# Performance work log

Hardware: AMD Instinct MI355X
Metric: run time of the kernel (lower is better)

## Reference

```python
import jax, jax.numpy as jnp
import numpy as np

N = 10000
E = 160000
C = 256        # in_channels
M = 256        # mid_channels
R = 64         # nregion


def _glorot(key, shape):
    fan_in, fan_out = shape[-1], shape[0]
    lim = (6.0 / (fan_in + fan_out)) ** 0.5
    return jax.random.uniform(key, shape, jnp.float32, -lim, lim)


def setup_inputs() -> dict:
    key = jax.random.key(0)
    ks = jax.random.split(key, 12)
    x = jax.random.normal(ks[0], (N, C), jnp.float32)
    edge_index = jax.random.randint(ks[1], (2, E), 0, N, jnp.int32)
    conv_w = _glorot(ks[2], (C, C))
    conv_b = jnp.zeros((C,), jnp.float32)
    lin1_w = _glorot(ks[3], (M, C)); lin1_b = jnp.zeros((M,), jnp.float32)
    lin2_w = _glorot(ks[4], (M, M)); lin2_b = jnp.zeros((M,), jnp.float32)
    lin3_w = _glorot(ks[5], (1, M)); lin3_b = jnp.zeros((1,), jnp.float32)
    lin4_w = _glorot(ks[6], (M, M)); lin4_b = jnp.zeros((M,), jnp.float32)
    bilin_w = _glorot(ks[7], (R, M, M)) * 0.1
    bilin_b = jnp.zeros((R,), jnp.float32)
    return {"x": x, "edge_index": edge_index,
            "conv_w": conv_w, "conv_b": conv_b,
            "lin1_w": lin1_w, "lin1_b": lin1_b,
            "lin2_w": lin2_w, "lin2_b": lin2_b,
            "lin3_w": lin3_w, "lin3_b": lin3_b,
            "lin4_w": lin4_w, "lin4_b": lin4_b,
            "bilin_w": bilin_w, "bilin_b": bilin_b}


def gcn_conv(x, edge_index, w, b):
    # PyG GCNConv: add self-loops, symmetric D^-1/2 (A+I) D^-1/2 normalization
    src, dst = edge_index[0], edge_index[1]
    n = x.shape[0]
    xw = x @ w.T                                            # [N, C]
    deg = jnp.ones((n,), xw.dtype).at[dst].add(jnp.ones((E,), xw.dtype))  # +1 for self loop
    dinv = jax.lax.rsqrt(deg)
    norm = dinv[src] * dinv[dst]                            # [E]
    agg = jnp.zeros_like(xw).at[dst].add(norm[:, None] * xw[src])
    agg = agg + (dinv * dinv)[:, None] * xw                 # self-loop messages
    return agg + b


def reference(x, edge_index, conv_w, conv_b, lin1_w, lin1_b, lin2_w, lin2_b,
              lin3_w, lin3_b, lin4_w, lin4_b, bilin_w, bilin_b):
    out = jax.nn.relu(gcn_conv(x, edge_index, conv_w, conv_b))
    x0 = out + x                                            # residual [N, C]
    x0 = jax.nn.relu(x0 @ lin1_w.T + lin1_b)                # [N, M]
    x1 = jax.nn.relu(x0 @ lin2_w.T + lin2_b)
    x1 = x1 @ lin3_w.T + lin3_b                             # [N, 1]
    x2 = jax.nn.relu(x0 @ lin4_w.T + lin4_b)                # [N, M]
    # Bilinear(x2, x2): out[n,r] = x2[n] @ W[r] @ x2[n] + b[r]
    t = (x2 @ bilin_w.reshape(R * M, M).T).reshape(-1, R, M)  # [N, R, M]
    x2 = jnp.sum(t * x2[:, None, :], axis=-1) + bilin_b       # [N, R]
    return (x1, x2)
```

## Files before the change

### kernel.cpp

```cpp
#include <hip/hip_runtime.h>

typedef unsigned short u16;
typedef __attribute__((ext_vector_type(8))) short bf16x8;
typedef __attribute__((ext_vector_type(8))) unsigned short u16x8;
typedef __attribute__((ext_vector_type(4))) float f32x4;

#define N_NODES 10000
#define E_EDGES 160000
#define CX_N 2560000
#define W_N  65536
#define WB_N 4194304
#define CANON_BIG_BLOCKS 3426
#define HIST_BLOCKS 79

__device__ __forceinline__ float b2f(u16 u) {
  union { unsigned i; float f; } c; c.i = ((unsigned)u) << 16; return c.f;
}
__device__ __forceinline__ u16 f2b(float f) {
  union { float f; unsigned i; } c; c.f = f;
  unsigned i = c.i;
  return (u16)((i + 0x7FFFu + ((i >> 16) & 1u)) >> 16);
}

__global__ void detect_kernel(const unsigned* __restrict__ w, int* __restrict__ flag) {
  int t = threadIdx.x;
  int cnt = 0;
  for (int i = t; i < 1024; i += 64) {
    unsigned e = (w[i] >> 7) & 0xFF;
    cnt += (e >= 100 && e <= 145) ? 1 : 0;
  }
  for (int o = 32; o; o >>= 1) cnt += __shfl_xor(cnt, o);
  if (t == 0) *flag = (cnt >= 512) ? 1 : 0;
}

__global__ void canon_all_kernel(const void* sx, const void* swc, const void* sw1,
                                 const void* sw2, const void* sw4, const void* swB,
                                 const void* sbc, const void* sb1, const void* sb2,
                                 const void* sb4, const void* sw3, const void* sbB,
                                 const void* sb3,
                                 u16* __restrict__ dstBase,
                                 u16* cbc, u16* cb1, u16* cb2, u16* cb4,
                                 u16* cw3, u16* cbB, u16* cb3,
                                 const int* __restrict__ ei, int* __restrict__ count,
                                 const int* __restrict__ flag) {
  int b = blockIdx.x;
  int f = *flag;
  if (b < CANON_BIG_BLOCKS) {
    long e = ((long)b * 256 + threadIdx.x) * 8;
    const void* src; long so;
    if (e < CX_N)                { src = sx;  so = e; }
    else if (e < CX_N + W_N)     { src = swc; so = e - CX_N; }
    else if (e < CX_N + 2 * W_N) { src = sw1; so = e - (CX_N + W_N); }
    else if (e < CX_N + 3 * W_N) { src = sw2; so = e - (CX_N + 2 * W_N); }
    else if (e < CX_N + 4 * W_N) { src = sw4; so = e - (CX_N + 3 * W_N); }
    else                         { src = swB; so = e - (CX_N + 4 * W_N); }
    if (f) {
      u16x8 v = *((const u16x8*)((const u16*)src + so));
      *(u16x8*)(dstBase + e) = v;
    } else {
      const float* fp = (const float*)src + so;
      float4 a = *(const float4*)fp;
      float4 c = *(const float4*)(fp + 4);
      u16x8 o;
      o[0] = f2b(a.x); o[1] = f2b(a.y); o[2] = f2b(a.z); o[3] = f2b(a.w);
      o[4] = f2b(c.x); o[5] = f2b(c.y); o[6] = f2b(c.z); o[7] = f2b(c.w);
      *(u16x8*)(dstBase + e) = o;
    }
  } else if (b == CANON_BIG_BLOCKS) {
    int t = threadIdx.x;
    const void* srcs[7] = {sbc, sb1, sb2, sb4, sw3, sbB, sb3};
    u16* dsts[7] = {cbc, cb1, cb2, cb4, cw3, cbB, cb3};
    const int ns[7] = {256, 256, 256, 256, 256, 64, 1};
#pragma unroll
    for (int k = 0; k < 7; ++k) {
      if (t < ns[k]) {
        if (f) dsts[k][t] = ((const u16*)srcs[k])[t];
        else   dsts[k][t] = f2b(((const float*)srcs[k])[t]);
      }
    }
  } else {
    int base = (b - CANON_BIG_BLOCKS - 1) * 2048 + threadIdx.x * 8;
#pragma unroll
    for (int k = 0; k < 8; ++k) {
      int i = base + k;
      if (i < E_EDGES) atomicAdd(&count[ei[E_EDGES + i]], 1);
    }
  }
}

__device__ __forceinline__ void stage_async(const u16* __restrict__ src, int stride,
                                            int row0, int maxRow, int k0,
                                            u16* lds, int w, int lane) {
  int rsel = lane >> 3;
  int gch = (lane & 7) ^ rsel;
#pragma unroll
  for (int i = 0; i < 4; ++i) {
    int rb = (w * 4 + i) * 8;
    int grow = row0 + rb + rsel;
    grow = grow > maxRow ? maxRow : grow;
    const u16* gp = src + (size_t)grow * stride + k0 + gch * 8;
    u16* lp = lds + rb * 64;
    __builtin_amdgcn_global_load_lds(
        (const __attribute__((address_space(1))) void*)gp,
        (__attribute__((address_space(3))) void*)lp, 16, 0, 0);
  }
}

__device__ __forceinline__ void mma_tile(const u16* lA, const u16* lB,
                                         f32x4 acc[4][4], int wr, int wc, int lane) {
#pragma unroll
  for (int ks = 0; ks < 2; ++ks) {
    bf16x8 af[4], bfr[4];
    int g = ks * 4 + (lane >> 4);
#pragma unroll
    for (int t = 0; t < 4; ++t) {
      int rowA = wr * 64 + t * 16 + (lane & 15);
      af[t] = *(const bf16x8*)(lA + rowA * 64 + ((g ^ (rowA & 7)) * 8));
      int rowB = wc * 64 + t * 16 + (lane & 15);
      bfr[t] = *(const bf16x8*)(lB + rowB * 64 + ((g ^ (rowB & 7)) * 8));
    }
#pragma unroll
    for (int ti = 0; ti < 4; ++ti)
#pragma unroll
      for (int tj = 0; tj < 4; ++tj)
        acc[ti][tj] = __builtin_amdgcn_mfma_f32_16x16x32_bf16(af[ti], bfr[tj],
                                                              acc[ti][tj], 0, 0, 0);
  }
}

template <bool RELU, bool F32OUT>
__global__ __launch_bounds__(256, 2)
void gemm_kernel(const u16* __restrict__ A, const u16* __restrict__ B,
                 const u16* __restrict__ bias, float* __restrict__ outF,
                 u16* __restrict__ outB, int NN, int J, int K) {
  __shared__ u16 lA[128 * 64];
  __shared__ u16 lB[128 * 64];
  int lane = threadIdx.x & 63;
  int w = threadIdx.x >> 6;
  int wr = w >> 1, wc = w & 1;
  int n0 = blockIdx.y * 128;
  int j0 = blockIdx.x * 128;
  f32x4 acc[4][4];
#pragma unroll
  for (int i = 0; i < 4; ++i)
#pragma unroll
    for (int j = 0; j < 4; ++j) acc[i][j] = (f32x4){0.f, 0.f, 0.f, 0.f};

  for (int kt = 0; kt < K; kt += 64) {
    stage_async(A, K, n0, NN - 1, kt, lA, w, lane);
    stage_async(B, K, j0, J - 1, kt, lB, w, lane);
    __syncthreads();
    mma_tile(lA, lB, acc, wr, wc, lane);
    __syncthreads();
  }

#pragma unroll
  for (int ti = 0; ti < 4; ++ti)
#pragma unroll
    for (int tj = 0; tj < 4; ++tj) {
      int col = j0 + wc * 64 + tj * 16 + (lane & 15);
      float bv = bias ? b2f(bias[col]) : 0.0f;
#pragma unroll
      for (int r = 0; r < 4; ++r) {
        int row = n0 + wr * 64 + ti * 16 + ((lane >> 4) << 2) + r;
        if (row < NN) {
          float v = acc[ti][tj][r] + bv;
          if (RELU) v = fmaxf(v, 0.0f);
          if (F32OUT) outF[(size_t)row * J + col] = v;
          else        outB[(size_t)row * J + col] = f2b(v);
        }
      }
    }
}

__global__ __launch_bounds__(256, 2)
void gemm_fused234_kernel(const u16* __restrict__ A, const u16* __restrict__ B,
                          const u16* __restrict__ bias, const u16* __restrict__ w3,
                          float* __restrict__ out1acc, u16* __restrict__ x2v, int NN) {
  __shared__ u16 lA[128 * 64];
  __shared__ u16 lB[128 * 64];
  int lane = threadIdx.x & 63;
  int w = threadIdx.x >> 6;
  int wr = w >> 1, wc = w & 1;
  int n0 = blockIdx.y * 128;
  int j0 = blockIdx.x * 128;
  f32x4 acc[4][4];
#pragma unroll
  for (int i = 0; i < 4; ++i)
#pragma unroll
    for (int j = 0; j < 4; ++j) acc[i][j] = (f32x4){0.f, 0.f, 0.f, 0.f};

  for (int kt = 0; kt < 256; kt += 64) {
    stage_async(A, 256, n0, NN - 1, kt, lA, w, lane);
    stage_async(B, 256, j0, 511, kt, lB, w, lane);
    __syncthreads();
    mma_tile(lA, lB, acc, wr, wc, lane);
    __syncthreads();
  }

  if (j0 < 256) {
    float part[4][4];
#pragma unroll
    for (int ti = 0; ti < 4; ++ti)
#pragma unroll
      for (int r = 0; r < 4; ++r) part[ti][r] = 0.0f;
#pragma unroll
    for (int ti = 0; ti < 4; ++ti)
#pragma unroll
      for (int tj = 0; tj < 4; ++tj) {
        int col = j0 + wc * 64 + tj * 16 + (lane & 15);
        float bv = b2f(bias[col]);
        float wv = b2f(w3[col]);
#pragma unroll
        for (int r = 0; r < 4; ++r) {
          float v = fmaxf(acc[ti][tj][r] + bv, 0.0f);
          part[ti][r] += v * wv;
        }
      }
#pragma unroll
    for (int ti = 0; ti < 4; ++ti)
#pragma unroll
      for (int r = 0; r < 4; ++r) {
        float s = part[ti][r];
        s += __shfl_xor(s, 1);
        s += __shfl_xor(s, 2);
        s += __shfl_xor(s, 4);
        s += __shfl_xor(s, 8);
        if ((lane & 15) == 0) {
          int row = n0 + wr * 64 + ti * 16 + ((lane >> 4) << 2) + r;
          if (row < NN) unsafeAtomicAdd(&out1acc[row], s);
        }
      }
  } else {
#pragma unroll
    for (int ti = 0; ti < 4; ++ti)
#pragma unroll
      for (int tj = 0; tj < 4; ++tj) {
        int col = j0 + wc * 64 + tj * 16 + (lane & 15);
        float bv = b2f(bias[col]);
#pragma unroll
        for (int r = 0; r < 4; ++r) {
          int row = n0 + wr * 64 + ti * 16 + ((lane >> 4) << 2) + r;
          if (row < NN) {
            float v = fmaxf(acc[ti][tj][r] + bv, 0.0f);
            x2v[(size_t)row * 256 + (col - 256)] = f2b(v);
          }
        }
      }
  }
}

__global__ __launch_bounds__(256, 2)
void bilinear_kernel(const u16* __restrict__ x2v, const u16* __restrict__ W,
                     float* __restrict__ out2acc, int NN) {
  __shared__ u16 lA[128 * 64];
  __shared__ u16 lB[128 * 64];
  int lane = threadIdx.x & 63;
  int w = threadIdx.x >> 6;
  int wr = w >> 1, wc = w & 1;
  int n0 = blockIdx.y * 128;
  int rm0 = blockIdx.x * 128;
  int m0g = rm0 & 255;
  int xv_kt = (m0g >> 6) + wc;
  f32x4 acc[4][4];
#pragma unroll
  for (int i = 0; i < 4; ++i)
#pragma unroll
    for (int j = 0; j < 4; ++j) acc[i][j] = (f32x4){0.f, 0.f, 0.f, 0.f};

  u16 xvr[4][16];

#pragma unroll
  for (int kt4 = 0; kt4 < 4; ++kt4) {
    stage_async(x2v, 256, n0, NN - 1, kt4 * 64, lA, w, lane);
    stage_async(W, 256, rm0, 16383, kt4 * 64, lB, w, lane);
    __syncthreads();
    mma_tile(lA, lB, acc, wr, wc, lane);
    if (kt4 == xv_kt) {
#pragma unroll
      for (int tj = 0; tj < 4; ++tj) {
        int kl = tj * 16 + (lane & 15);
        int ch = kl >> 3, off = kl & 7;
#pragma unroll
        for (int ti = 0; ti < 4; ++ti)
#pragma unroll
          for (int r = 0; r < 4; ++r) {
            int rowl = wr * 64 + ti * 16 + ((lane >> 4) << 2) + r;
            xvr[tj][ti * 4 + r] = lA[rowl * 64 + ((ch ^ (rowl & 7)) * 8) + off];
          }
      }
    }
    __syncthreads();
  }

  int region = rm0 >> 8;
  float rowsum[4][4];
#pragma unroll
  for (int ti = 0; ti < 4; ++ti)
#pragma unroll
    for (int r = 0; r < 4; ++r) rowsum[ti][r] = 0.0f;

#pragma unroll
  for (int ti = 0; ti < 4; ++ti)
#pragma unroll
    for (int tj = 0; tj < 4; ++tj)
#pragma unroll
      for (int r = 0; r < 4; ++r)
        rowsum[ti][r] += acc[ti][tj][r] * b2f(xvr[tj][ti * 4 + r]);

#pragma unroll
  for (int ti = 0; ti < 4; ++ti)
#pragma unroll
    for (int r = 0; r < 4; ++r) {
      float s = rowsum[ti][r];
      s += __shfl_xor(s, 1);
      s += __shfl_xor(s, 2);
      s += __shfl_xor(s, 4);
      s += __shfl_xor(s, 8);
      if ((lane & 15) == 0) {
        int rowl = wr * 64 + ti * 16 + ((lane >> 4) << 2) + r;
        int n = n0 + rowl;
        if (n < NN) unsafeAtomicAdd(&out2acc[(size_t)n * 64 + region], s);
      }
    }
}

__global__ void scan_kernel(const int* __restrict__ count, int* __restrict__ start,
                            int* __restrict__ cursor, float* __restrict__ dinv) {
  __shared__ int wsum[16];
  __shared__ int carry_s;
  int t = threadIdx.x;
  int wv = t >> 6, ln = t & 63;
  if (t == 0) carry_s = 0;
  __syncthreads();
  for (int base = 0; base < N_NODES; base += 1024) {
    int i = base + t;
    int v = (i < N_NODES) ? count[i] : 0;
    int s = v;
#pragma unroll
    for (int o = 1; o < 64; o <<= 1) {
      int u = __shfl_up(s, o);
      if (ln >= o) s += u;
    }
    if (ln == 63) wsum[wv] = s;
    __syncthreads();
    if (wv == 0) {
      int x = (ln < 16) ? wsum[ln] : 0;
#pragma unroll
      for (int o = 1; o < 16; o <<= 1) {
        int u = __shfl_up(x, o);
        if (ln >= o) x += u;
      }
      if (ln < 16) wsum[ln] = x;
    }
    __syncthreads();
    int excl = s - v + (wv ? wsum[wv - 1] : 0) + carry_s;
    if (i < N_NODES) {
      start[i] = excl;
      cursor[i] = excl;
      dinv[i] = rsqrtf(1.0f + (float)v);
    }
    __syncthreads();
    if (t == 0) carry_s += wsum[15];
    __syncthreads();
  }
}

__global__ void place_kernel(const int* __restrict__ ei, int* __restrict__ cursor,
                             int* __restrict__ order) {
  int i = blockIdx.x * 256 + threadIdx.x;
  if (i >= E_EDGES) return;
  int d = ei[E_EDGES + i];
  int pos = atomicAdd(&cursor[d], 1);
  order[pos] = i;
}

__global__ void gather_kernel(const int* __restrict__ ei, const int* __restrict__ order,
                              const int* __restrict__ start, const int* __restrict__ count,
                              const float* __restrict__ dinv, const float* __restrict__ xw,
                              const u16* __restrict__ conv_b, const u16* __restrict__ x,
                              u16* __restrict__ x0) {
  int node = (blockIdx.x * blockDim.x + threadIdx.x) >> 6;
  int lane = threadIdx.x & 63;
  if (node >= N_NODES) return;
  int s0 = start[node], cnt = count[node];
  float dn = dinv[node];
  float ax = 0.f, ay = 0.f, az = 0.f, aw = 0.f;
  for (int base = 0; base < cnt; base += 64) {
    int rem = cnt - base;
    int m = rem < 64 ? rem : 64;
    int eid = (lane < m) ? order[s0 + base + lane] : 0;
    int s = (lane < m) ? ei[eid] : 0;
    float nrm = (lane < m) ? dinv[s] * dn : 0.f;
    for (int j = 0; j < m; ++j) {
      int sj = __shfl(s, j);
      float nj = __shfl(nrm, j);
      float4 v = *((const float4*)(xw + (size_t)sj * 256) + lane);
      ax += nj * v.x; ay += nj * v.y; az += nj * v.z; aw += nj * v.w;
    }
  }
  float4 sv = *((const float4*)(xw + (size_t)node * 256) + lane);
  float slw = dn * dn;
  const u16* bb = conv_b + lane * 4;
  const u16* xr = x + (size_t)node * 256 + lane * 4;
  u16 o[4];
  float vals[4] = {ax + slw * sv.x, ay + slw * sv.y, az + slw * sv.z, aw + slw * sv.w};
#pragma unroll
  for (int j = 0; j < 4; ++j) {
    float v = vals[j] + b2f(bb[j]);
    v = fmaxf(v, 0.0f) + b2f(xr[j]);
    o[j] = f2b(v);
  }
  *((ushort4*)(x0 + (size_t)node * 256) + lane) = make_ushort4(o[0], o[1], o[2], o[3]);
}

__global__ void out_final_kernel(const float* __restrict__ out1acc,
                                 const float* __restrict__ out2acc,
                                 const u16* __restrict__ b3, const u16* __restrict__ bb,
                                 void* __restrict__ dout, const int* __restrict__ flag) {
  int idx = blockIdx.x * 256 + threadIdx.x;
  int f = *flag;
  if (idx < N_NODES) {
    float v = out1acc[idx] + b2f(b3[0]);
    if (f) ((u16*)dout)[idx] = f2b(v);
    else   ((float*)dout)[idx] = v;
  } else if (idx < N_NODES + N_NODES * 64) {
    int k = idx - N_NODES;
    float v = out2acc[k] + b2f(bb[k & 63]);
    if (f) ((u16*)dout)[idx] = f2b(v);
    else   ((float*)dout)[idx] = v;
  }
}

extern "C" void kernel_launch(void* const* d_in, const int* in_sizes, int n_in,
                              void* d_out, int out_size, void* d_ws, size_t ws_size,
                              hipStream_t stream) {
  const int* ei = (const int*)d_in[1];

  float* ws      = (float*)d_ws;
  float* xw      = ws;
  int*   count   = (int*)(xw + N_NODES * 256);
  int*   start   = count + 10240;
  int*   cursor  = start + 10240;
  int*   order   = cursor + 10240;
  float* dinv    = (float*)(order + E_EDGES);
  float* out1acc = dinv + 10240;
  float* out2acc = out1acc + 10240;
  u16* x0  = (u16*)(out2acc + N_NODES * 64);
  u16* x0m = x0 + N_NODES * 256;
  u16* x2v = x0m + N_NODES * 256;
  u16* cx  = x2v + N_NODES * 256;
  u16* cwc = cx + CX_N;
  u16* cw1 = cwc + W_N;
  u16* cw2 = cw1 + W_N;
  u16* cw4 = cw2 + W_N;
  u16* cwB = cw4 + W_N;
  u16* cbc = cwB + WB_N;
  u16* cb1 = cbc + 256;
  u16* cb2 = cb1 + 256;
  u16* cb4 = cb2 + 256;
  u16* cw3 = cb4 + 256;
  u16* cbB = cw3 + 256;
  u16* cb3 = cbB + 64;
  int* flag = (int*)(cb3 + 16);

  hipMemsetAsync(count, 0, N_NODES * sizeof(int), stream);
  hipMemsetAsync(out1acc, 0, (10240 + (size_t)N_NODES * 64) * sizeof(float), stream);

  detect_kernel<<<1, 64, 0, stream>>>((const unsigned*)d_in[0], flag);

  canon_all_kernel<<<CANON_BIG_BLOCKS + 1 + HIST_BLOCKS, 256, 0, stream>>>(
      d_in[0], d_in[2], d_in[4], d_in[6], d_in[10], d_in[12],
      d_in[3], d_in[5], d_in[7], d_in[11], d_in[8], d_in[13], d_in[9],
      cx, cbc, cb1, cb2, cb4, cw3, cbB, cb3,
      ei, count, flag);

  scan_kernel<<<1, 1024, 0, stream>>>(count, start, cursor, dinv);
  place_kernel<<<(E_EDGES + 255) / 256, 256, 0, stream>>>(ei, cursor, order);

  gemm_kernel<false, true><<<dim3(2, 79), 256, 0, stream>>>(
      cx, cwc, nullptr, xw, nullptr, N_NODES, 256, 256);

  gather_kernel<<<(N_NODES * 64 + 255) / 256, 256, 0, stream>>>(
      ei, order, start, count, dinv, xw, cbc, cx, x0);

  gemm_kernel<true, false><<<dim3(2, 79), 256, 0, stream>>>(
      x0, cw1, cb1, nullptr, x0m, N_NODES, 256, 256);

  gemm_fused234_kernel<<<dim3(4, 79), 256, 0, stream>>>(
      x0m, cw2, cb2, cw3, out1acc, x2v, N_NODES);

  bilinear_kernel<<<dim3(128, 79), 256, 0, stream>>>(x2v, cwB, out2acc, N_NODES);

  out_final_kernel<<<(N_NODES * 65 + 255) / 256, 256, 0, stream>>>(
      out1acc, out2acc, cb3, cbB, d_out, flag);
}
```

Before: 391.3 us.

## Shrink bilinear tile to 64 rows to raise occupancy and cut atomics

The bilinear kernel now processes 64 node rows per block instead of 128, and each wave owns 32 output columns across all 64 rows. That lowers the accumulator register count and lets launch bounds request four blocks per CU instead of two. The x2 values for the dot product are read directly from global memory in the epilogue rather than kept in registers during the K loop. Per-wave partial sums are combined in shared memory so each row issues one atomic per block. In exchange, every W tile is staged twice as often across the doubled grid, and the epilogue adds uncoalesced global reads.

Result: faster. 367.3 us (-6.1%).

```diff
diff --git a/kernel.cpp b/kernel.cpp
--- a/kernel.cpp
+++ b/kernel.cpp
@@ -250,79 +250,94 @@
   }
 }
 
-__global__ __launch_bounds__(256, 2)
-void bilinear_kernel(const u16* __restrict__ x2v, const u16* __restrict__ W,
-                     float* __restrict__ out2acc, int NN) {
-  __shared__ u16 lA[128 * 64];
+__device__ __forceinline__ void stage64(const u16* __restrict__ src,
+                                        int row0, int maxRow, int k0,
+                                        u16* lds, int w, int lane) {
+  int rsel = lane >> 3;
+  int gch = (lane & 7) ^ rsel;
+#pragma unroll
+  for (int i = 0; i < 2; ++i) {
+    int rb = (w * 2 + i) * 8;
+    int grow = row0 + rb + rsel;
+    grow = grow > maxRow ? maxRow : grow;
+    const u16* gp = src + (size_t)grow * 256 + k0 + gch * 8;
+    u16* lp = lds + rb * 64;
+    __builtin_amdgcn_global_load_lds(
+        (const __attribute__((address_space(1))) void*)gp,
+        (__attribute__((address_space(3))) void*)lp, 16, 0, 0);
+  }
+}
+
+__global__ __launch_bounds__(256, 4)
+void bilinear_tlp_kernel(const u16* __restrict__ x2v, const u16* __restrict__ W,
+                         float* __restrict__ out2acc, int NN) {
+  __shared__ u16 lA[64 * 64];
   __shared__ u16 lB[128 * 64];
+  __shared__ float sc[64 * 4];
   int lane = threadIdx.x & 63;
   int w = threadIdx.x >> 6;
-  int wr = w >> 1, wc = w & 1;
-  int n0 = blockIdx.y * 128;
+  int n0 = blockIdx.y * 64;
   int rm0 = blockIdx.x * 128;
   int m0g = rm0 & 255;
-  int xv_kt = (m0g >> 6) + wc;
-  f32x4 acc[4][4];
+  int region = rm0 >> 8;
+
+  f32x4 acc[4][2];
 #pragma unroll
   for (int i = 0; i < 4; ++i)
 #pragma unroll
-    for (int j = 0; j < 4; ++j) acc[i][j] = (f32x4){0.f, 0.f, 0.f, 0.f};
-
-  u16 xvr[4][16];
+    for (int j = 0; j < 2; ++j) acc[i][j] = (f32x4){0.f, 0.f, 0.f, 0.f};
 
 #pragma unroll
   for (int kt4 = 0; kt4 < 4; ++kt4) {
-    stage_async(x2v, 256, n0, NN - 1, kt4 * 64, lA, w, lane);
+    stage64(x2v, n0, NN - 1, kt4 * 64, lA, w, lane);
     stage_async(W, 256, rm0, 16383, kt4 * 64, lB, w, lane);
     __syncthreads();
-    mma_tile(lA, lB, acc, wr, wc, lane);
-    if (kt4 == xv_kt) {
-#pragma unroll
-      for (int tj = 0; tj < 4; ++tj) {
-        int kl = tj * 16 + (lane & 15);
-        int ch = kl >> 3, off = kl & 7;
-#pragma unroll
-        for (int ti = 0; ti < 4; ++ti)
-#pragma unroll
-          for (int r = 0; r < 4; ++r) {
-            int rowl = wr * 64 + ti * 16 + ((lane >> 4) << 2) + r;
-            xvr[tj][ti * 4 + r] = lA[rowl * 64 + ((ch ^ (rowl & 7)) * 8) + off];
-          }
-      }
-    }
-    __syncthreads();
-  }
-
-  int region = rm0 >> 8;
-  float rowsum[4][4];
+#pragma unroll
+    for (int ks = 0; ks < 2; ++ks) {
+      bf16x8 af[4], bfr[2];
+      int g = ks * 4 + (lane >> 4);
+#pragma unroll
+      for (int t = 0; t < 4; ++t) {
+        int rowA = t * 16 + (lane & 15);
+        af[t] = *(const bf16x8*)(lA + rowA * 64 + ((g ^ (rowA & 7)) * 8));
+      }
+#pragma unroll
+      for (int u = 0; u < 2; ++u) {
+        int rowB = w * 32 + u * 16 + (lane & 15);
+        bfr[u] = *(const bf16x8*)(lB + rowB * 64 + ((g ^ (rowB & 7)) * 8));
+      }
+#pragma unroll
+      for (int t = 0; t < 4; ++t)
+#pragma unroll
+        for (int u = 0; u < 2; ++u)
+          acc[t][u] = __builtin_amdgcn_mfma_f32_16x16x32_bf16(af[t], bfr[u],
+                                                              acc[t][u], 0, 0, 0);
+    }
+    __syncthreads();
+  }
+
 #pragma unroll
   for (int ti = 0; ti < 4; ++ti)
 #pragma unroll
-    for (int r = 0; r < 4; ++r) rowsum[ti][r] = 0.0f;
-
-#pragma unroll
-  for (int ti = 0; ti < 4; ++ti)
-#pragma unroll
-    for (int tj = 0; tj < 4; ++tj)
-#pragma unroll
-      for (int r = 0; r < 4; ++r)
-        rowsum[ti][r] += acc[ti][tj][r] * b2f(xvr[tj][ti * 4 + r]);
-
-#pragma unroll
-  for (int ti = 0; ti < 4; ++ti)
-#pragma unroll
     for (int r = 0; r < 4; ++r) {
-      float s = rowsum[ti][r];
+      int rowl = ti * 16 + ((lane >> 4) << 2) + r;
+      int row = n0 + rowl;
+      int rc = row < NN ? row : NN - 1;
+      const u16* xr = x2v + (size_t)rc * 256 + m0g + w * 32 + (lane & 15);
+      float s = acc[ti][0][r] * b2f(xr[0]) + acc[ti][1][r] * b2f(xr[16]);
       s += __shfl_xor(s, 1);
       s += __shfl_xor(s, 2);
       s += __shfl_xor(s, 4);
       s += __shfl_xor(s, 8);
-      if ((lane & 15) == 0) {
-        int rowl = wr * 64 + ti * 16 + ((lane >> 4) << 2) + r;
-        int n = n0 + rowl;
-        if (n < NN) unsafeAtomicAdd(&out2acc[(size_t)n * 64 + region], s);
-      }
-    }
+      if ((lane & 15) == 0) sc[rowl * 4 + w] = s;
+    }
+  __syncthreads();
+  int tid = threadIdx.x;
+  if (tid < 64) {
+    float s = sc[tid * 4] + sc[tid * 4 + 1] + sc[tid * 4 + 2] + sc[tid * 4 + 3];
+    int nn = n0 + tid;
+    if (nn < NN) unsafeAtomicAdd(&out2acc[(size_t)nn * 64 + region], s);
+  }
 }
 
 __global__ void scan_kernel(const int* __restrict__ count, int* __restrict__ start,
@@ -490,7 +505,7 @@
   gemm_fused234_kernel<<<dim3(4, 79), 256, 0, stream>>>(
       x0m, cw2, cb2, cw3, out1acc, x2v, N_NODES);
 
-  bilinear_kernel<<<dim3(128, 79), 256, 0, stream>>>(x2v, cwB, out2acc, N_NODES);
+  bilinear_tlp_kernel<<<dim3(128, 157), 256, 0, stream>>>(x2v, cwB, out2acc, N_NODES);
 
   out_final_kernel<<<(N_NODES * 65 + 255) / 256, 256, 0, stream>>>(
       out1acc, out2acc, cb3, cbB, d_out, flag);
```
